# Optimization experiments

Hardware: AMD Instinct MI355X
Metric: run time of the kernel (lower is better)

The kernel has to match this reference:

```python
import jax, jax.numpy as jnp
import numpy as np

N_NODES = 100000
N_EDGES = 1600000
IN_DIM = 128
HID = 128
OUT = 40


def setup_inputs() -> dict:
    key = jax.random.key(0)
    ks = jax.random.split(key, 8)
    x = jax.random.normal(ks[0], (N_NODES, IN_DIM), dtype=jnp.float32)
    edge_index = jax.random.randint(ks[1], (2, N_EDGES), 0, N_NODES, dtype=jnp.int64)
    def glorot(k, fan_in, fan_out):
        s = jnp.sqrt(6.0 / (fan_in + fan_out)).astype(jnp.float32)
        return jax.random.uniform(k, (fan_in, fan_out), jnp.float32, -s, s)
    return {
        "x": x,
        "edge_index": edge_index,
        "W1": glorot(ks[2], IN_DIM, HID), "b1": jnp.zeros((HID,), jnp.float32),
        "W2": glorot(ks[3], HID, HID),    "b2": jnp.zeros((HID,), jnp.float32),
        "W3": glorot(ks[4], HID, HID),    "b3": jnp.zeros((HID,), jnp.float32),
        "Wl": glorot(ks[5], HID, OUT),    "bl": jnp.zeros((OUT,), jnp.float32),
    }


def _gcn_norm(edge_index, num_nodes):
    # PyG GCNConv default: add self-loops, symmetric normalization.
    loops = jnp.arange(num_nodes, dtype=edge_index.dtype)
    src = jnp.concatenate([edge_index[0], loops])
    dst = jnp.concatenate([edge_index[1], loops])
    deg = jax.ops.segment_sum(jnp.ones_like(dst, dtype=jnp.float32), dst,
                              num_segments=num_nodes)
    dis = jnp.where(deg > 0, jax.lax.rsqrt(deg), 0.0)  # deg^{-1/2}
    norm = dis[src] * dis[dst]  # [E+N]
    return src, dst, norm


def _gcn_conv(x, W, b, src, dst, norm, num_nodes):
    h = x @ W                                   # [N, F_out]
    msg = h[src] * norm[:, None]                # gather + scale
    out = jax.ops.segment_sum(msg, dst, num_segments=num_nodes)
    return out + b


def reference(x, edge_index, W1, b1, W2, b2, W3, b3, Wl, bl):
    n = x.shape[0]
    src, dst, norm = _gcn_norm(edge_index, n)
    h = jax.nn.relu(_gcn_conv(x, W1, b1, src, dst, norm, n))
    h = jax.nn.relu(_gcn_conv(h, W2, b2, src, dst, norm, n))
    h = _gcn_conv(h, W3, b3, src, dst, norm, n)
    # dropout p=0.5 is identity in eval mode
    return h @ Wl + bl
```

## Files before the change

### kernel.cpp

```cpp
#include <hip/hip_runtime.h>

typedef __attribute__((ext_vector_type(8))) short sh8;
typedef __attribute__((ext_vector_type(4))) float f4;

__device__ __forceinline__ float bf2f(unsigned short u) {
    union { unsigned int u; float f; } c; c.u = ((unsigned int)u) << 16; return c.f;
}
__device__ __forceinline__ unsigned short f2bf(float f) {
    union { float f; unsigned int u; } c; c.f = f;
    unsigned int x = c.u;
    unsigned int r = (x + 0x7fffu + ((x >> 16) & 1u)) >> 16;
    return (unsigned short)r;
}
__device__ __forceinline__ void bfsplit(float x, short& hi, short& lo) {
    unsigned short h = f2bf(x);
    float r = x - bf2f(h);
    hi = (short)h;
    lo = (short)f2bf(r);
}

#define CSR_GRID 1568

__global__ void k_zero_cnt(int* cnt, int M) {
    int i = blockIdx.x * 256 + threadIdx.x;
    if (i < M) cnt[i] = 0;
}

__global__ void k_count(const int* __restrict__ dst, int* __restrict__ cnt8,
                        int* __restrict__ rank, int E, int N) {
    int base = (blockIdx.x & 7) * N;
    int E4 = E >> 2;
    for (int i = blockIdx.x * 256 + threadIdx.x; i < E4; i += gridDim.x * 256) {
        int4 d = ((const int4*)dst)[i];
        int4 r;
        r.x = ((unsigned)d.x < (unsigned)N) ? atomicAdd(&cnt8[base + d.x], 1) : -1;
        r.y = ((unsigned)d.y < (unsigned)N) ? atomicAdd(&cnt8[base + d.y], 1) : -1;
        r.z = ((unsigned)d.z < (unsigned)N) ? atomicAdd(&cnt8[base + d.z], 1) : -1;
        r.w = ((unsigned)d.w < (unsigned)N) ? atomicAdd(&cnt8[base + d.w], 1) : -1;
        ((int4*)rank)[i] = r;
    }
    if (blockIdx.x == 0) {
        for (int e = (E4 << 2) + threadIdx.x; e < E; e += 256) {
            int d = dst[e];
            rank[e] = ((unsigned)d < (unsigned)N) ? atomicAdd(&cnt8[d], 1) : -1;
        }
    }
}

#define SCAN_B 256
__global__ void k_scan_a(const int* __restrict__ cnt8, int* __restrict__ rowptr,
                         int* __restrict__ off8, int* __restrict__ deg,
                         int* __restrict__ bsum, float* __restrict__ dis, int N) {
    __shared__ int sh[SCAN_B];
    int t = threadIdx.x, i = blockIdx.x * SCAN_B + t;
    int c[8];
    int v = 0;
    if (i < N) {
        #pragma unroll
        for (int g = 0; g < 8; ++g) { c[g] = cnt8[g * N + i]; v += c[g]; }
        dis[i] = rsqrtf((float)(v + 1));
        deg[i] = v;
    }
    sh[t] = v; __syncthreads();
    for (int off = 1; off < SCAN_B; off <<= 1) {
        int x = (t >= off) ? sh[t - off] : 0;
        __syncthreads();
        sh[t] += x;
        __syncthreads();
    }
    int incl = sh[t];
    if (i < N) {
        int b = incl - v;
        rowptr[i] = b;
        int o = b;
        #pragma unroll
        for (int g = 0; g < 8; ++g) { off8[g * N + i] = o; o += c[g]; }
    }
    if (t == SCAN_B - 1) bsum[blockIdx.x] = incl;
}

__global__ void k_scan_b(int* bsum, int NB) {
    __shared__ int sh[512];
    int t = threadIdx.x;
    int v = (t < NB) ? bsum[t] : 0;
    sh[t] = v; __syncthreads();
    for (int off = 1; off < 512; off <<= 1) {
        int x = (t >= off) ? sh[t - off] : 0;
        __syncthreads();
        sh[t] += x;
        __syncthreads();
    }
    if (t < NB) bsum[t] = sh[t] - v;
}

__global__ void k_scan_c(int* __restrict__ rowptr, int* __restrict__ off8,
                         const int* __restrict__ bsum, int N) {
    int i = blockIdx.x * 256 + threadIdx.x;
    if (i < N) {
        int b = bsum[blockIdx.x];
        rowptr[i] += b;
        #pragma unroll
        for (int g = 0; g < 8; ++g) off8[g * N + i] += b;
    }
}

__global__ void k_fill(const int* __restrict__ src, const int* __restrict__ dst,
                       const int* __restrict__ rank, const int* __restrict__ off8,
                       int* __restrict__ csrc, int E, int N) {
    int E4 = E >> 2;
    for (int i = blockIdx.x * 256 + threadIdx.x; i < E4; i += gridDim.x * 256) {
        int g = ((i >> 8) % gridDim.x) & 7;
        const int* off = off8 + g * N;
        int4 d4 = ((const int4*)dst)[i];
        int4 s4 = ((const int4*)src)[i];
        int4 r4 = ((const int4*)rank)[i];
        #pragma unroll
        for (int q = 0; q < 4; ++q) {
            int d = (q == 0) ? d4.x : (q == 1) ? d4.y : (q == 2) ? d4.z : d4.w;
            int s = (q == 0) ? s4.x : (q == 1) ? s4.y : (q == 2) ? s4.z : s4.w;
            int r = (q == 0) ? r4.x : (q == 1) ? r4.y : (q == 2) ? r4.z : r4.w;
            if ((unsigned)d >= (unsigned)N || (unsigned)s >= (unsigned)N || r < 0) continue;
            csrc[off[d] + r] = s;
        }
    }
    if (blockIdx.x == 0) {
        for (int e = (E4 << 2) + threadIdx.x; e < E; e += 256) {
            int d = dst[e];
            int s = src[e];
            int r = rank[e];
            if ((unsigned)d >= (unsigned)N || (unsigned)s >= (unsigned)N || r < 0) continue;
            csrc[off8[d] + r] = s;
        }
    }
}

__global__ __launch_bounds__(256)
void k_gemm128_a32(const float* __restrict__ X,
                   const float* __restrict__ W,
                   const float* __restrict__ dis,
                   unsigned short* __restrict__ H, int nPairs) {
    int wave = threadIdx.x >> 6;
    int lane = threadIdx.x & 63;
    int ln = lane & 15, quad = lane >> 4;
    int c0 = (wave & 1) * 64;
    int subTile = wave >> 1;

    sh8 bh[4][4], blo[4][4];
    #pragma unroll
    for (int nt = 0; nt < 4; ++nt) {
        int col = c0 + nt * 16 + ln;
        #pragma unroll
        for (int kt = 0; kt < 4; ++kt) {
            int k0 = kt * 32 + quad * 8;
            #pragma unroll
            for (int j = 0; j < 8; ++j) {
                short h, l;
                bfsplit(W[(k0 + j) * 128 + col], h, l);
                bh[nt][kt][j] = h; blo[nt][kt][j] = l;
            }
        }
    }

    for (int p = blockIdx.x; p < nPairs; p += gridDim.x) {
        int nodeBase = p * 32 + subTile * 16;
        const float* xrow = X + (nodeBase + ln) * 128 + quad * 8;
        sh8 ah[4], al[4];
        #pragma unroll
        for (int kt = 0; kt < 4; ++kt) {
            f4 v0 = *(const f4*)(xrow + kt * 32);
            f4 v1 = *(const f4*)(xrow + kt * 32 + 4);
            #pragma unroll
            for (int j = 0; j < 4; ++j) {
                short h, l;
                bfsplit(v0[j], h, l); ah[kt][j] = h; al[kt][j] = l;
                bfsplit(v1[j], h, l); ah[kt][j + 4] = h; al[kt][j + 4] = l;
            }
        }

        f4 acc[4] = { {0.f,0.f,0.f,0.f}, {0.f,0.f,0.f,0.f}, {0.f,0.f,0.f,0.f}, {0.f,0.f,0.f,0.f} };
        #pragma unroll
        for (int kt = 0; kt < 4; ++kt)
            #pragma unroll
            for (int nt = 0; nt < 4; ++nt) {
                acc[nt] = __builtin_amdgcn_mfma_f32_16x16x32_bf16(ah[kt], bh[nt][kt], acc[nt], 0, 0, 0);
                acc[nt] = __builtin_amdgcn_mfma_f32_16x16x32_bf16(ah[kt], blo[nt][kt], acc[nt], 0, 0, 0);
                acc[nt] = __builtin_amdgcn_mfma_f32_16x16x32_bf16(al[kt], bh[nt][kt], acc[nt], 0, 0, 0);
            }

        float ds[4];
        #pragma unroll
        for (int r = 0; r < 4; ++r) ds[r] = dis[nodeBase + quad * 4 + r];
        #pragma unroll
        for (int nt = 0; nt < 4; ++nt) {
            int col = c0 + nt * 16 + ln;
            #pragma unroll
            for (int r = 0; r < 4; ++r)
                H[(nodeBase + quad * 4 + r) * 128 + col] = f2bf(acc[nt][r] * ds[r]);
        }
    }
}

__global__ __launch_bounds__(256)
void k_gemm128_a16(const unsigned short* __restrict__ X,
                   const float* __restrict__ W,
                   const float* __restrict__ dis,
                   unsigned short* __restrict__ H, int nPairs) {
    int wave = threadIdx.x >> 6;
    int lane = threadIdx.x & 63;
    int ln = lane & 15, quad = lane >> 4;
    int c0 = (wave & 1) * 64;
    int subTile = wave >> 1;

    sh8 bh[4][4], blo[4][4];
    #pragma unroll
    for (int nt = 0; nt < 4; ++nt) {
        int col = c0 + nt * 16 + ln;
        #pragma unroll
        for (int kt = 0; kt < 4; ++kt) {
            int k0 = kt * 32 + quad * 8;
            #pragma unroll
            for (int j = 0; j < 8; ++j) {
                short h, l;
                bfsplit(W[(k0 + j) * 128 + col], h, l);
                bh[nt][kt][j] = h; blo[nt][kt][j] = l;
            }
        }
    }

    for (int p = blockIdx.x; p < nPairs; p += gridDim.x) {
        int nodeBase = p * 32 + subTile * 16;
        const unsigned short* xrow = X + (nodeBase + ln) * 128 + quad * 8;
        sh8 a[4];
        #pragma unroll
        for (int kt = 0; kt < 4; ++kt) a[kt] = *(const sh8*)(xrow + kt * 32);

        f4 acc[4] = { {0.f,0.f,0.f,0.f}, {0.f,0.f,0.f,0.f}, {0.f,0.f,0.f,0.f}, {0.f,0.f,0.f,0.f} };
        #pragma unroll
        for (int kt = 0; kt < 4; ++kt)
            #pragma unroll
            for (int nt = 0; nt < 4; ++nt) {
                acc[nt] = __builtin_amdgcn_mfma_f32_16x16x32_bf16(a[kt], bh[nt][kt], acc[nt], 0, 0, 0);
                acc[nt] = __builtin_amdgcn_mfma_f32_16x16x32_bf16(a[kt], blo[nt][kt], acc[nt], 0, 0, 0);
            }

        float ds[4];
        #pragma unroll
        for (int r = 0; r < 4; ++r) ds[r] = dis[nodeBase + quad * 4 + r];
        #pragma unroll
        for (int nt = 0; nt < 4; ++nt) {
            int col = c0 + nt * 16 + ln;
            #pragma unroll
            for (int r = 0; r < 4; ++r)
                H[(nodeBase + quad * 4 + r) * 128 + col] = f2bf(acc[nt][r] * ds[r]);
        }
    }
}

__global__ __launch_bounds__(256)
void k_agg(const unsigned short* __restrict__ H,
           unsigned short* __restrict__ O,
           const float* __restrict__ dis,
           const int* __restrict__ rowptr,
           const int* __restrict__ deg,
           const int* __restrict__ csrc,
           const float* __restrict__ bias,
           int relu, int N) {
    int n = (blockIdx.x * 256 + threadIdx.x) >> 5;
    if (n >= N) return;
    int lane = threadIdx.x & 31;
    int sub  = lane & 15;
    int half = lane >> 4;

    float a0 = 0.f, a1 = 0.f, a2 = 0.f, a3 = 0.f;
    float a4 = 0.f, a5 = 0.f, a6 = 0.f, a7 = 0.f;

    auto addrow = [&](uint4 v) {
        a0 += bf2f((unsigned short)v.x);
        a1 += bf2f((unsigned short)(v.x >> 16));
        a2 += bf2f((unsigned short)v.y);
        a3 += bf2f((unsigned short)(v.y >> 16));
        a4 += bf2f((unsigned short)v.z);
        a5 += bf2f((unsigned short)(v.z >> 16));
        a6 += bf2f((unsigned short)v.w);
        a7 += bf2f((unsigned short)(v.w >> 16));
    };

    if (half == 0)
        addrow(*(const uint4*)(H + (size_t)n * 128 + sub * 8));

    int start = rowptr[n];
    int e = deg[n];
    int i = 0;
    for (; i + 8 <= e; i += 8) {
        int s[4];
        #pragma unroll
        for (int q = 0; q < 4; ++q) s[q] = csrc[start + i + 2 * q + half];
        uint4 v[4];
        #pragma unroll
        for (int q = 0; q < 4; ++q) v[q] = *(const uint4*)(H + (size_t)s[q] * 128 + sub * 8);
        #pragma unroll
        for (int q = 0; q < 4; ++q) addrow(v[q]);
    }
    for (int j = i + half; j < e; j += 2) {
        int s = csrc[start + j];
        addrow(*(const uint4*)(H + (size_t)s * 128 + sub * 8));
    }

    a0 += __shfl_xor(a0, 16); a1 += __shfl_xor(a1, 16);
    a2 += __shfl_xor(a2, 16); a3 += __shfl_xor(a3, 16);
    a4 += __shfl_xor(a4, 16); a5 += __shfl_xor(a5, 16);
    a6 += __shfl_xor(a6, 16); a7 += __shfl_xor(a7, 16);

    if (half == 0) {
        float dn = dis[n];
        f4 b0 = *(const f4*)(bias + sub * 8);
        f4 b1 = *(const f4*)(bias + sub * 8 + 4);
        a0 = a0 * dn + b0[0]; a1 = a1 * dn + b0[1];
        a2 = a2 * dn + b0[2]; a3 = a3 * dn + b0[3];
        a4 = a4 * dn + b1[0]; a5 = a5 * dn + b1[1];
        a6 = a6 * dn + b1[2]; a7 = a7 * dn + b1[3];
        if (relu) {
            a0 = fmaxf(a0, 0.f); a1 = fmaxf(a1, 0.f);
            a2 = fmaxf(a2, 0.f); a3 = fmaxf(a3, 0.f);
            a4 = fmaxf(a4, 0.f); a5 = fmaxf(a5, 0.f);
            a6 = fmaxf(a6, 0.f); a7 = fmaxf(a7, 0.f);
        }
        uint4 ov;
        ov.x = (unsigned int)f2bf(a0) | ((unsigned int)f2bf(a1) << 16);
        ov.y = (unsigned int)f2bf(a2) | ((unsigned int)f2bf(a3) << 16);
        ov.z = (unsigned int)f2bf(a4) | ((unsigned int)f2bf(a5) << 16);
        ov.w = (unsigned int)f2bf(a6) | ((unsigned int)f2bf(a7) << 16);
        *(uint4*)(O + (size_t)n * 128 + sub * 8) = ov;
    }
}

__global__ __launch_bounds__(256)
void k_gemm_final(const unsigned short* __restrict__ X,
                  const float* __restrict__ W,
                  const float* __restrict__ bl,
                  float* __restrict__ OUT, int nTiles) {
    int wave = threadIdx.x >> 6;
    int lane = threadIdx.x & 63;
    int ln = lane & 15, quad = lane >> 4;
    int tile = blockIdx.x * 4 + wave;
    if (tile >= nTiles) return;

    sh8 bh[3][4], blo[3][4];
    #pragma unroll
    for (int nt = 0; nt < 3; ++nt) {
        int col = nt * 16 + ln;
        bool valid = (col < 40);
        #pragma unroll
        for (int kt = 0; kt < 4; ++kt) {
            int k0 = kt * 32 + quad * 8;
            #pragma unroll
            for (int j = 0; j < 8; ++j) {
                short h = 0, l = 0;
                if (valid) bfsplit(W[(k0 + j) * 40 + col], h, l);
                bh[nt][kt][j] = h; blo[nt][kt][j] = l;
            }
        }
    }

    int nodeBase = tile * 16;
    const unsigned short* xrow = X + (nodeBase + ln) * 128 + quad * 8;
    sh8 a[4];
    #pragma unroll
    for (int kt = 0; kt < 4; ++kt) a[kt] = *(const sh8*)(xrow + kt * 32);

    f4 acc[3] = { {0.f,0.f,0.f,0.f}, {0.f,0.f,0.f,0.f}, {0.f,0.f,0.f,0.f} };
    #pragma unroll
    for (int kt = 0; kt < 4; ++kt)
        #pragma unroll
        for (int nt = 0; nt < 3; ++nt) {
            acc[nt] = __builtin_amdgcn_mfma_f32_16x16x32_bf16(a[kt], bh[nt][kt], acc[nt], 0, 0, 0);
            acc[nt] = __builtin_amdgcn_mfma_f32_16x16x32_bf16(a[kt], blo[nt][kt], acc[nt], 0, 0, 0);
        }

    #pragma unroll
    for (int nt = 0; nt < 3; ++nt) {
        int col = nt * 16 + ln;
        if (col < 40) {
            float bv = bl[col];
            #pragma unroll
            for (int r = 0; r < 4; ++r)
                OUT[(nodeBase + quad * 4 + r) * 40 + col] = acc[nt][r] + bv;
        }
    }
}

extern "C" void kernel_launch(void* const* d_in, const int* in_sizes, int n_in,
                              void* d_out, int out_size, void* d_ws, size_t ws_size,
                              hipStream_t stream) {
    const float* x  = (const float*)d_in[0];
    const int*   ei = (const int*)d_in[1];
    const float* W1 = (const float*)d_in[2];
    const float* b1 = (const float*)d_in[3];
    const float* W2 = (const float*)d_in[4];
    const float* b2 = (const float*)d_in[5];
    const float* W3 = (const float*)d_in[6];
    const float* b3 = (const float*)d_in[7];
    const float* Wl = (const float*)d_in[8];
    const float* bl = (const float*)d_in[9];

    const int N = in_sizes[0] / 128;
    const int E = in_sizes[1] / 2;
    const int* srcIdx = ei;
    const int* dstIdx = ei + E;

    char* ws = (char*)d_ws;
    size_t off = 0;
    auto alloc = [&](size_t bytes) { void* p = ws + off; off += (bytes + 511) & ~(size_t)511; return p; };
    int*   rowptr  = (int*)  alloc((size_t)N * 4);
    int*   deg     = (int*)  alloc((size_t)N * 4);
    float* dis     = (float*)alloc((size_t)N * 4);
    int*   bsum    = (int*)  alloc(512 * 4);
    int*   csrc    = (int*)  alloc((size_t)E * 4);
    unsigned short* h0 = (unsigned short*)alloc((size_t)N * 128 * 2);
    unsigned short* h1 = (unsigned short*)alloc((size_t)N * 128 * 2);
    int* rank = (int*)h0;
    int* cnt8 = (int*)((char*)h0 + (8u << 20));
    int* off8 = (int*)h1;

    const int gN = (N + 255) / 256;
    const int nPairs = N / 32;
    const int nTiles = N / 16;
    const int gAgg = (N * 32 + 255) / 256;
    const int gZ8 = (N * 8 + 255) / 256;

    k_zero_cnt<<<gZ8, 256, 0, stream>>>(cnt8, N * 8);
    k_count<<<CSR_GRID, 256, 0, stream>>>(dstIdx, cnt8, rank, E, N);
    k_scan_a<<<gN, 256, 0, stream>>>(cnt8, rowptr, off8, deg, bsum, dis, N);
    k_scan_b<<<1, 512, 0, stream>>>(bsum, gN);
    k_scan_c<<<gN, 256, 0, stream>>>(rowptr, off8, bsum, N);
    k_fill<<<CSR_GRID, 256, 0, stream>>>(srcIdx, dstIdx, rank, off8, csrc, E, N);

    k_gemm128_a32<<<768, 256, 0, stream>>>(x, W1, dis, h0, nPairs);
    k_agg<<<gAgg, 256, 0, stream>>>(h0, h1, dis, rowptr, deg, csrc, b1, 1, N);
    k_gemm128_a16<<<768, 256, 0, stream>>>(h1, W2, dis, h0, nPairs);
    k_agg<<<gAgg, 256, 0, stream>>>(h0, h1, dis, rowptr, deg, csrc, b2, 1, N);
    k_gemm128_a16<<<768, 256, 0, stream>>>(h1, W3, dis, h0, nPairs);
    k_agg<<<gAgg, 256, 0, stream>>>(h0, h1, dis, rowptr, deg, csrc, b3, 0, N);
    k_gemm_final<<<(nTiles + 3) / 4, 256, 0, stream>>>(h1, Wl, bl, (float*)d_out, nTiles);
}
```

Before: 492.9 us.

## Co-schedule edge counting with first GEMM in one launch; defer dis scaling

The first-layer GEMM no longer depends on the degree normalization, so it is merged with the edge-count kernel into a single launch where even blocks count and odd blocks run the GEMM. The source-side dis scaling for layer one moves into the aggregation, which now loads dis per neighbor and uses an FMA. Scratch buffers are remapped to h1 so the GEMM output in h0 is not clobbered. The aim is to overlap the atomic-bound counting with the compute-bound GEMM and drop one launch, at the cost of extra gathers of dis in the first aggregation.

```diff
diff --git a/kernel.cpp b/kernel.cpp
--- a/kernel.cpp
+++ b/kernel.cpp
@@ -19,18 +19,23 @@
     lo = (short)f2bf(r);
 }
 
-#define CSR_GRID 1568
+#define CG_BLOCKS 2304
+#define CG_COUNT  1152
+#define CSR_GRID  1568
 
 __global__ void k_zero_cnt(int* cnt, int M) {
     int i = blockIdx.x * 256 + threadIdx.x;
     if (i < M) cnt[i] = 0;
 }
 
-__global__ void k_count(const int* __restrict__ dst, int* __restrict__ cnt8,
-                        int* __restrict__ rank, int E, int N) {
-    int base = (blockIdx.x & 7) * N;
+
+__device__ __forceinline__ void count_body(const int* __restrict__ dst,
+                                           int* __restrict__ cnt8,
+                                           int* __restrict__ rank, int E, int N) {
+    int cidx = blockIdx.x >> 1;
+    int base = (cidx & 7) * N;
     int E4 = E >> 2;
-    for (int i = blockIdx.x * 256 + threadIdx.x; i < E4; i += gridDim.x * 256) {
+    for (int i = cidx * 256 + threadIdx.x; i < E4; i += CG_COUNT * 256) {
         int4 d = ((const int4*)dst)[i];
         int4 r;
         r.x = ((unsigned)d.x < (unsigned)N) ? atomicAdd(&cnt8[base + d.x], 1) : -1;
@@ -39,12 +44,85 @@
         r.w = ((unsigned)d.w < (unsigned)N) ? atomicAdd(&cnt8[base + d.w], 1) : -1;
         ((int4*)rank)[i] = r;
     }
-    if (blockIdx.x == 0) {
+    if (cidx == 0) {
         for (int e = (E4 << 2) + threadIdx.x; e < E; e += 256) {
             int d = dst[e];
             rank[e] = ((unsigned)d < (unsigned)N) ? atomicAdd(&cnt8[d], 1) : -1;
         }
     }
+}
+
+__device__ __forceinline__ void gemm1_body(const float* __restrict__ X,
+                                           const float* __restrict__ W,
+                                           unsigned short* __restrict__ H, int nPairs) {
+    int gidx = blockIdx.x >> 1;
+    int wave = threadIdx.x >> 6;
+    int lane = threadIdx.x & 63;
+    int ln = lane & 15, quad = lane >> 4;
+    int c0 = (wave & 1) * 64;
+    int subTile = wave >> 1;
+
+    sh8 bh[4][4], blo[4][4];
+    #pragma unroll
+    for (int nt = 0; nt < 4; ++nt) {
+        int col = c0 + nt * 16 + ln;
+        #pragma unroll
+        for (int kt = 0; kt < 4; ++kt) {
+            int k0 = kt * 32 + quad * 8;
+            #pragma unroll
+            for (int j = 0; j < 8; ++j) {
+                short h, l;
+                bfsplit(W[(k0 + j) * 128 + col], h, l);
+                bh[nt][kt][j] = h; blo[nt][kt][j] = l;
+            }
+        }
+    }
+
+    for (int p = gidx; p < nPairs; p += CG_COUNT) {
+        int nodeBase = p * 32 + subTile * 16;
+        const float* xrow = X + (nodeBase + ln) * 128 + quad * 8;
+        sh8 ah[4], al[4];
+        #pragma unroll
+        for (int kt = 0; kt < 4; ++kt) {
+            f4 v0 = *(const f4*)(xrow + kt * 32);
+            f4 v1 = *(const f4*)(xrow + kt * 32 + 4);
+            #pragma unroll
+            for (int j = 0; j < 4; ++j) {
+                short h, l;
+                bfsplit(v0[j], h, l); ah[kt][j] = h; al[kt][j] = l;
+                bfsplit(v1[j], h, l); ah[kt][j + 4] = h; al[kt][j + 4] = l;
+            }
+        }
+
+        f4 acc[4] = { {0.f,0.f,0.f,0.f}, {0.f,0.f,0.f,0.f}, {0.f,0.f,0.f,0.f}, {0.f,0.f,0.f,0.f} };
+        #pragma unroll
+        for (int kt = 0; kt < 4; ++kt)
+            #pragma unroll
+            for (int nt = 0; nt < 4; ++nt) {
+                acc[nt] = __builtin_amdgcn_mfma_f32_16x16x32_bf16(ah[kt], bh[nt][kt], acc[nt], 0, 0, 0);
+                acc[nt] = __builtin_amdgcn_mfma_f32_16x16x32_bf16(ah[kt], blo[nt][kt], acc[nt], 0, 0, 0);
+                acc[nt] = __builtin_amdgcn_mfma_f32_16x16x32_bf16(al[kt], bh[nt][kt], acc[nt], 0, 0, 0);
+            }
+
+        #pragma unroll
+        for (int nt = 0; nt < 4; ++nt) {
+            int col = c0 + nt * 16 + ln;
+            #pragma unroll
+            for (int r = 0; r < 4; ++r)
+                H[(nodeBase + quad * 4 + r) * 128 + col] = f2bf(acc[nt][r]);
+        }
+    }
+}
+
+__global__ __launch_bounds__(256)
+void k_count_gemm1(const int* __restrict__ dst, int* __restrict__ cnt8,
+                   int* __restrict__ rank, int E, int N,
+                   const float* __restrict__ X, const float* __restrict__ W,
+                   unsigned short* __restrict__ H, int nPairs) {
+    if ((blockIdx.x & 1) == 0)
+        count_body(dst, cnt8, rank, E, N);
+    else
+        gemm1_body(X, W, H, nPairs);
 }
 
 #define SCAN_B 256
@@ -109,7 +187,7 @@
                        int* __restrict__ csrc, int E, int N) {
     int E4 = E >> 2;
     for (int i = blockIdx.x * 256 + threadIdx.x; i < E4; i += gridDim.x * 256) {
-        int g = ((i >> 8) % gridDim.x) & 7;
+        int g = (i >> 8) & 7;
         const int* off = off8 + g * N;
         int4 d4 = ((const int4*)dst)[i];
         int4 s4 = ((const int4*)src)[i];
@@ -130,72 +208,6 @@
             int r = rank[e];
             if ((unsigned)d >= (unsigned)N || (unsigned)s >= (unsigned)N || r < 0) continue;
             csrc[off8[d] + r] = s;
-        }
-    }
-}
-
-__global__ __launch_bounds__(256)
-void k_gemm128_a32(const float* __restrict__ X,
-                   const float* __restrict__ W,
-                   const float* __restrict__ dis,
-                   unsigned short* __restrict__ H, int nPairs) {
-    int wave = threadIdx.x >> 6;
-    int lane = threadIdx.x & 63;
-    int ln = lane & 15, quad = lane >> 4;
-    int c0 = (wave & 1) * 64;
-    int subTile = wave >> 1;
-
-    sh8 bh[4][4], blo[4][4];
-    #pragma unroll
-    for (int nt = 0; nt < 4; ++nt) {
-        int col = c0 + nt * 16 + ln;
-        #pragma unroll
-        for (int kt = 0; kt < 4; ++kt) {
-            int k0 = kt * 32 + quad * 8;
-            #pragma unroll
-            for (int j = 0; j < 8; ++j) {
-                short h, l;
-                bfsplit(W[(k0 + j) * 128 + col], h, l);
-                bh[nt][kt][j] = h; blo[nt][kt][j] = l;
-            }
-        }
-    }
-
-    for (int p = blockIdx.x; p < nPairs; p += gridDim.x) {
-        int nodeBase = p * 32 + subTile * 16;
-        const float* xrow = X + (nodeBase + ln) * 128 + quad * 8;
-        sh8 ah[4], al[4];
-        #pragma unroll
-        for (int kt = 0; kt < 4; ++kt) {
-            f4 v0 = *(const f4*)(xrow + kt * 32);
-            f4 v1 = *(const f4*)(xrow + kt * 32 + 4);
-            #pragma unroll
-            for (int j = 0; j < 4; ++j) {
-                short h, l;
-                bfsplit(v0[j], h, l); ah[kt][j] = h; al[kt][j] = l;
-                bfsplit(v1[j], h, l); ah[kt][j + 4] = h; al[kt][j + 4] = l;
-            }
-        }
-
-        f4 acc[4] = { {0.f,0.f,0.f,0.f}, {0.f,0.f,0.f,0.f}, {0.f,0.f,0.f,0.f}, {0.f,0.f,0.f,0.f} };
-        #pragma unroll
-        for (int kt = 0; kt < 4; ++kt)
-            #pragma unroll
-            for (int nt = 0; nt < 4; ++nt) {
-                acc[nt] = __builtin_amdgcn_mfma_f32_16x16x32_bf16(ah[kt], bh[nt][kt], acc[nt], 0, 0, 0);
-                acc[nt] = __builtin_amdgcn_mfma_f32_16x16x32_bf16(ah[kt], blo[nt][kt], acc[nt], 0, 0, 0);
-                acc[nt] = __builtin_amdgcn_mfma_f32_16x16x32_bf16(al[kt], bh[nt][kt], acc[nt], 0, 0, 0);
-            }
-
-        float ds[4];
-        #pragma unroll
-        for (int r = 0; r < 4; ++r) ds[r] = dis[nodeBase + quad * 4 + r];
-        #pragma unroll
-        for (int nt = 0; nt < 4; ++nt) {
-            int col = c0 + nt * 16 + ln;
-            #pragma unroll
-            for (int r = 0; r < 4; ++r)
-                H[(nodeBase + quad * 4 + r) * 128 + col] = f2bf(acc[nt][r] * ds[r]);
         }
     }
 }
@@ -264,7 +276,7 @@
            const int* __restrict__ deg,
            const int* __restrict__ csrc,
            const float* __restrict__ bias,
-           int relu, int N) {
+           int relu, int scaled, int N) {
     int n = (blockIdx.x * 256 + threadIdx.x) >> 5;
     if (n >= N) return;
     int lane = threadIdx.x & 31;
@@ -273,6 +285,7 @@
 
     float a0 = 0.f, a1 = 0.f, a2 = 0.f, a3 = 0.f;
     float a4 = 0.f, a5 = 0.f, a6 = 0.f, a7 = 0.f;
+    float dn = dis[n];
 
     auto addrow = [&](uint4 v) {
         a0 += bf2f((unsigned short)v.x);
@@ -284,26 +297,59 @@
         a6 += bf2f((unsigned short)v.w);
         a7 += bf2f((unsigned short)(v.w >> 16));
     };
-
-    if (half == 0)
-        addrow(*(const uint4*)(H + (size_t)n * 128 + sub * 8));
+    auto addroww = [&](uint4 v, float w) {
+        a0 = fmaf(w, bf2f((unsigned short)v.x), a0);
+        a1 = fmaf(w, bf2f((unsigned short)(v.x >> 16)), a1);
+        a2 = fmaf(w, bf2f((unsigned short)v.y), a2);
+        a3 = fmaf(w, bf2f((unsigned short)(v.y >> 16)), a3);
+        a4 = fmaf(w, bf2f((unsigned short)v.z), a4);
+        a5 = fmaf(w, bf2f((unsigned short)(v.z >> 16)), a5);
+        a6 = fmaf(w, bf2f((unsigned short)v.w), a6);
+        a7 = fmaf(w, bf2f((unsigned short)(v.w >> 16)), a7);
+    };
+
+    if (half == 0) {
+        uint4 v = *(const uint4*)(H + (size_t)n * 128 + sub * 8);
+        if (scaled) addrow(v); else addroww(v, dn);
+    }
 
     int start = rowptr[n];
     int e = deg[n];
     int i = 0;
-    for (; i + 8 <= e; i += 8) {
-        int s[4];
-        #pragma unroll
-        for (int q = 0; q < 4; ++q) s[q] = csrc[start + i + 2 * q + half];
-        uint4 v[4];
-        #pragma unroll
-        for (int q = 0; q < 4; ++q) v[q] = *(const uint4*)(H + (size_t)s[q] * 128 + sub * 8);
-        #pragma unroll
-        for (int q = 0; q < 4; ++q) addrow(v[q]);
-    }
-    for (int j = i + half; j < e; j += 2) {
-        int s = csrc[start + j];
-        addrow(*(const uint4*)(H + (size_t)s * 128 + sub * 8));
+    if (scaled) {
+        for (; i + 8 <= e; i += 8) {
+            int s[4];
+            #pragma unroll
+            for (int q = 0; q < 4; ++q) s[q] = csrc[start + i + 2 * q + half];
+            uint4 v[4];
+            #pragma unroll
+            for (int q = 0; q < 4; ++q) v[q] = *(const uint4*)(H + (size_t)s[q] * 128 + sub * 8);
+            #pragma unroll
+            for (int q = 0; q < 4; ++q) addrow(v[q]);
+        }
+        for (int j = i + half; j < e; j += 2) {
+            int s = csrc[start + j];
+            addrow(*(const uint4*)(H + (size_t)s * 128 + sub * 8));
+        }
+    } else {
+        for (; i + 8 <= e; i += 8) {
+            int s[4];
+            #pragma unroll
+            for (int q = 0; q < 4; ++q) s[q] = csrc[start + i + 2 * q + half];
+            uint4 v[4];
+            #pragma unroll
+            for (int q = 0; q < 4; ++q) v[q] = *(const uint4*)(H + (size_t)s[q] * 128 + sub * 8);
+            float w[4];
+            #pragma unroll
+            for (int q = 0; q < 4; ++q) w[q] = dis[s[q]];
+            #pragma unroll
+            for (int q = 0; q < 4; ++q) addroww(v[q], w[q]);
+        }
+        for (int j = i + half; j < e; j += 2) {
+            int s = csrc[start + j];
+            float w = dis[s];
+            addroww(*(const uint4*)(H + (size_t)s * 128 + sub * 8), w);
+        }
     }
 
     a0 += __shfl_xor(a0, 16); a1 += __shfl_xor(a1, 16);
@@ -312,7 +358,6 @@
     a6 += __shfl_xor(a6, 16); a7 += __shfl_xor(a7, 16);
 
     if (half == 0) {
-        float dn = dis[n];
         f4 b0 = *(const f4*)(bias + sub * 8);
         f4 b1 = *(const f4*)(bias + sub * 8 + 4);
         a0 = a0 * dn + b0[0]; a1 = a1 * dn + b0[1];
@@ -418,9 +463,9 @@
     int*   csrc    = (int*)  alloc((size_t)E * 4);
     unsigned short* h0 = (unsigned short*)alloc((size_t)N * 128 * 2);
     unsigned short* h1 = (unsigned short*)alloc((size_t)N * 128 * 2);
-    int* rank = (int*)h0;
-    int* cnt8 = (int*)((char*)h0 + (8u << 20));
-    int* off8 = (int*)h1;
+    int* rank = (int*)h1;
+    int* off8 = (int*)((char*)h1 + (8u << 20));
+    int* cnt8 = (int*)((char*)h1 + (16u << 20));
 
     const int gN = (N + 255) / 256;
     const int nPairs = N / 32;
@@ -429,17 +474,17 @@
     const int gZ8 = (N * 8 + 255) / 256;
 
     k_zero_cnt<<<gZ8, 256, 0, stream>>>(cnt8, N * 8);
-    k_count<<<CSR_GRID, 256, 0, stream>>>(dstIdx, cnt8, rank, E, N);
+    k_count_gemm1<<<CG_BLOCKS, 256, 0, stream>>>(dstIdx, cnt8, rank, E, N,
+                                                 x, W1, h0, nPairs);
     k_scan_a<<<gN, 256, 0, stream>>>(cnt8, rowptr, off8, deg, bsum, dis, N);
     k_scan_b<<<1, 512, 0, stream>>>(bsum, gN);
     k_scan_c<<<gN, 256, 0, stream>>>(rowptr, off8, bsum, N);
     k_fill<<<CSR_GRID, 256, 0, stream>>>(srcIdx, dstIdx, rank, off8, csrc, E, N);
 
-    k_gemm128_a32<<<768, 256, 0, stream>>>(x, W1, dis, h0, nPairs);
-    k_agg<<<gAgg, 256, 0, stream>>>(h0, h1, dis, rowptr, deg, csrc, b1, 1, N);
+    k_agg<<<gAgg, 256, 0, stream>>>(h0, h1, dis, rowptr, deg, csrc, b1, 1, 0, N);
     k_gemm128_a16<<<768, 256, 0, stream>>>(h1, W2, dis, h0, nPairs);
-    k_agg<<<gAgg, 256, 0, stream>>>(h0, h1, dis, rowptr, deg, csrc, b2, 1, N);
+    k_agg<<<gAgg, 256, 0, stream>>>(h0, h1, dis, rowptr, deg, csrc, b2, 1, 1, N);
     k_gemm128_a16<<<768, 256, 0, stream>>>(h1, W3, dis, h0, nPairs);
-    k_agg<<<gAgg, 256, 0, stream>>>(h0, h1, dis, rowptr, deg, csrc, b3, 0, N);
+    k_agg<<<gAgg, 256, 0, stream>>>(h0, h1, dis, rowptr, deg, csrc, b3, 0, 1, N);
     k_gemm_final<<<(nTiles + 3) / 4, 256, 0, stream>>>(h1, Wl, bl, (float*)d_out, nTiles);
 }
```

Measured after the change: 479.1 us. 2.8% less time.
